# Kernel optimization log

Measured on AMD Instinct MI355X. Metric: run time of the kernel, lower is better.

## Reference

```python
import jax, jax.numpy as jnp
import numpy as np

B, NV, NRINGS, NDIRS, C, F = 2, 20000, 8, 8, 16, 16


def setup_inputs() -> dict:
    key = jax.random.key(0)
    ks = jax.random.split(key, 7)
    y = jax.random.normal(ks[0], (B, NV, NDIRS, C), jnp.float32)
    contributors = jax.random.randint(ks[1], (NV, NRINGS, NDIRS, 3), 0, NV, dtype=jnp.int32)
    weights_bary = jax.random.uniform(ks[2], (NV, NRINGS, NDIRS, 3), jnp.float32)
    angles = jax.random.randint(ks[3], (NV, NRINGS, NDIRS, 3), 0, NDIRS, dtype=jnp.int32)
    kernel = jax.random.normal(ks[4], (NRINGS, NDIRS, C, F), jnp.float32) * 0.05
    center_kernel = jax.random.normal(ks[5], (C, F), jnp.float32) * 0.05
    bias = jnp.zeros((F,), jnp.float32)
    return {"y": y, "contributors": contributors, "weights_bary": weights_bary,
            "angles": angles, "kernel": kernel, "center_kernel": center_kernel, "bias": bias}


def reference(y, contributors, weights_bary, angles, kernel, center_kernel, bias):
    # y: (B, nv, ndirs, C); tables: (nv, nrings, ndirs, 3)
    b, nv, ndirs, nch = y.shape
    nfilters = kernel.shape[-1]
    nrings = contributors.shape[1]

    # window_interpolation_sync: gather 3 contributor vertices per window bin,
    # with the direction axis re-indexed per-contributor (radial sync), then
    # barycentric-weighted sum.  Flatten (vertex, dir) into one gather index.
    idx = contributors * ndirs + angles                 # (nv, nrings, ndirs, 3)
    y_flat = y.reshape(b, nv * ndirs, nch)
    gathered = y_flat[:, idx, :]                        # (B, nv, nrings, ndirs, 3, C)
    z = jnp.einsum('bvrdjc,vrdj->bvrdc', gathered, weights_bary)  # (B, nv, nrings, ndirs, C)

    # gcnn_conv: circular pad over dirs then VALID conv with (nrings, ndirs) kernel
    zr = z.reshape(b * nv, nrings, ndirs, nch)
    zr = jnp.concatenate([zr, zr[:, :, :-1, :]], axis=2)  # width 2*ndirs-1
    conv = jax.lax.conv_general_dilated(
        zr, kernel, window_strides=(1, 1), padding='VALID',
        dimension_numbers=('NHWC', 'HWIO', 'NHWC'))       # (B*nv, 1, ndirs, F)
    conv = conv.reshape(b, nv, ndirs, nfilters)

    out = conv + jnp.einsum('bvdc,cf->bvdf', y, center_kernel) + bias
    out = jax.nn.relu(out)
    return jnp.max(out, axis=2)                          # take_max over directions -> (B, nv, F)
```

## Files before the change

### kernel.cpp

```cpp
#include <hip/hip_runtime.h>

typedef unsigned short u16;
typedef __attribute__((ext_vector_type(4))) unsigned int u32x4;
typedef __attribute__((ext_vector_type(4))) float f32x4;
typedef __attribute__((ext_vector_type(8))) __bf16 bf16x8;

constexpr int BATCH = 2;
constexpr int NV    = 20000;
constexpr int ND    = 8;
constexpr int CH    = 16;
constexpr int NF    = 16;
constexpr int NVD   = NV * ND;
constexpr int NCHUNK = 36;
constexpr int MTOT  = BATCH * NV;
constexpr int BSTR  = 40;
constexpr int KSPLIT_CH = 18;

constexpr size_t Y16_OFF_B = 0;
constexpr size_t K2C_OFF_B = 10240000;
constexpr size_t PB_OFF_B  = 10534912;

__device__ __forceinline__ u16 f2bf(float x) {
    unsigned int u = __float_as_uint(x);
    unsigned int r = (u + 0x7fffu + ((u >> 16) & 1u)) >> 16;
    return (u16)r;
}
__device__ __forceinline__ unsigned int pack2bf(float a, float b) {
    return (unsigned int)f2bf(a) | ((unsigned int)f2bf(b) << 16);
}

__global__ __launch_bounds__(256) void prep(const float* __restrict__ y,
                                            u16* __restrict__ y16) {
    int tid = blockIdx.x * 256 + threadIdx.x;
    const float4* src = (const float4*)(y + (size_t)tid * 16);
    float4 v0 = src[0], v1 = src[1], v2 = src[2], v3 = src[3];
    u32x4 lo = {pack2bf(v0.x, v0.y), pack2bf(v0.z, v0.w), pack2bf(v1.x, v1.y), pack2bf(v1.z, v1.w)};
    u32x4 hi = {pack2bf(v2.x, v2.y), pack2bf(v2.z, v2.w), pack2bf(v3.x, v3.y), pack2bf(v3.z, v3.w)};
    u16* yd = y16 + (size_t)tid * 16;
    *(u32x4*)(yd)     = lo;
    *(u32x4*)(yd + 8) = hi;
}

__global__ __launch_bounds__(256) void k2_build(const float* __restrict__ kern,
                                                const float* __restrict__ ck,
                                                u16* __restrict__ k2c) {
    int e = blockIdx.x * 256 + threadIdx.x;
    int i = e & 4095;
    int kc = e >> 12;
    int n = i >> 5, kk = i & 31;
    int k = kc * 32 + kk;
    int w = n >> 4, f = n & 15;
    float val;
    if (k < 1024) {
        int r = k >> 7, dd = (k >> 4) & 7, c = k & 15;
        int d = (dd - w) & 7;
        val = kern[((r * 8 + d) * 16 + c) * 16 + f];
    } else {
        int ke = k - 1024;
        int d = ke >> 4, c = ke & 15;
        val = (d == w) ? ck[c * 16 + f] : 0.f;
    }
    k2c[e] = f2bf(val);
}

__global__ __launch_bounds__(256) void fused_gather_gemm(const u16* __restrict__ y16,
                                                         const int* __restrict__ contrib,
                                                         const float* __restrict__ wbary,
                                                         const int* __restrict__ angles,
                                                         const u16* __restrict__ k2c,
                                                         float* __restrict__ pb) {
    __shared__ __align__(16) u16 Bb[2][128 * BSTR];
    const int t = threadIdx.x;
    const int s  = blockIdx.x & 1;
    const int kcBeg = s * KSPLIT_CH;
    const int kcEnd = kcBeg + KSPLIT_CH;
    const int w = t >> 6, lane = t & 63;
    const int lrow = lane & 15, lq = lane >> 4;
    const int s_p = lq >> 1;
    const int h8  = (lq & 1) * 8;
    const int m0 = (blockIdx.x >> 1) * 64;
    const int arow = m0 + w * 16 + lrow;
    const int b_p = (arow >= NV);
    const int v_p = arow - b_p * NV;
    const u16* __restrict__ yb = y16 + (size_t)b_p * NVD * CH + h8;
    const int mb0 = v_p * 192 + s_p * 3;
    const int sn = t >> 1, sh = (t & 1) * 16;

    int   ce0, ce1, ce2, ae0, ae1, ae2;  float we0, we1, we2;
    int   co0, co1, co2, ao0, ao1, ao2;  float wo0, wo1, wo2;
    u32x4 ge0, ge1, ge2;  float ve0, ve1, ve2;
    u32x4 go0, go1, go2;  float vo0, vo1, vo2;
    u32x4 bne0, bne1, bno0, bno1;

    f32x4 acc[8];
    #pragma unroll
    for (int nt = 0; nt < 8; ++nt) acc[nt] = (f32x4){0.f, 0.f, 0.f, 0.f};

#define META_ISSUE(S, KC_) { const int o_ = mb0 + (KC_) * 6;                       \
    c##S##0 = contrib[o_]; c##S##1 = contrib[o_ + 1]; c##S##2 = contrib[o_ + 2];   \
    a##S##0 = angles[o_];  a##S##1 = angles[o_ + 1];  a##S##2 = angles[o_ + 2];    \
    w##S##0 = wbary[o_];   w##S##1 = wbary[o_ + 1];   w##S##2 = wbary[o_ + 2]; }

#define G_ISSUE(S, KC_) {                                                          \
    if ((KC_) < 32) {                                                              \
        g##S##0 = *(const u32x4*)(yb + (size_t)((unsigned)c##S##0 * 128u +         \
                                                (unsigned)a##S##0 * 16u));         \
        g##S##1 = *(const u32x4*)(yb + (size_t)((unsigned)c##S##1 * 128u +         \
                                                (unsigned)a##S##1 * 16u));         \
        g##S##2 = *(const u32x4*)(yb + (size_t)((unsigned)c##S##2 * 128u +         \
                                                (unsigned)a##S##2 * 16u));         \
        v##S##0 = w##S##0; v##S##1 = w##S##1; v##S##2 = w##S##2;                   \
    } else {                                                                       \
        g##S##0 = *(const u32x4*)(yb + (size_t)((unsigned)v_p * 128u +             \
                                      (unsigned)(2 * ((KC_) - 32) + s_p) * 16u));  \
    } }

#define COMBINE(S, KC_, A_) {                                                      \
    if ((KC_) < 32) {                                                              \
        float ac_[8];                                                              \
        _Pragma("unroll") for (int x_ = 0; x_ < 8; ++x_) ac_[x_] = 0.f;            \
        _Pragma("unroll")                                                          \
        for (int q_ = 0; q_ < 4; ++q_) {                                           \
            unsigned u0_ = g##S##0[q_], u1_ = g##S##1[q_], u2_ = g##S##2[q_];      \
            ac_[2 * q_]     += v##S##0 * __uint_as_float(u0_ << 16);               \
            ac_[2 * q_ + 1] += v##S##0 * __uint_as_float(u0_ & 0xffff0000u);       \
            ac_[2 * q_]     += v##S##1 * __uint_as_float(u1_ << 16);               \
            ac_[2 * q_ + 1] += v##S##1 * __uint_as_float(u1_ & 0xffff0000u);       \
            ac_[2 * q_]     += v##S##2 * __uint_as_float(u2_ << 16);               \
            ac_[2 * q_ + 1] += v##S##2 * __uint_as_float(u2_ & 0xffff0000u);       \
        }                                                                          \
        u32x4 o_;                                                                  \
        _Pragma("unroll") for (int q_ = 0; q_ < 4; ++q_)                           \
            o_[q_] = pack2bf(ac_[2 * q_], ac_[2 * q_ + 1]);                        \
        A_ = *(bf16x8*)&o_;                                                        \
    } else { u32x4 o_ = g##S##0; A_ = *(bf16x8*)&o_; } }

    META_ISSUE(e, kcBeg); META_ISSUE(o, kcBeg + 1);
    {
        const u32x4* src = (const u32x4*)(k2c + (size_t)kcBeg * 4096 + sn * 32 + sh);
        u32x4 b0 = src[0], b1 = src[1];
        u16* dst = &Bb[0][sn * BSTR + sh];
        *(u32x4*)(dst)     = b0;
        *(u32x4*)(dst + 8) = b1;
    }
    G_ISSUE(e, kcBeg); META_ISSUE(e, kcBeg + 2);
    G_ISSUE(o, kcBeg + 1);
    {
        const u32x4* src = (const u32x4*)(k2c + (size_t)(kcBeg + 1) * 4096 + sn * 32 + sh);
        bno0 = src[0]; bno1 = src[1];
    }

    for (int p = 0; p < KSPLIT_CH / 2; ++p) {
        const int k0 = kcBeg + 2 * p, k1 = k0 + 1;

        __syncthreads();
        if (k0 + 2 < kcEnd) {
            const u32x4* src = (const u32x4*)(k2c + (size_t)(k0 + 2) * 4096 + sn * 32 + sh);
            bne0 = src[0]; bne1 = src[1];
        }
        bf16x8 aev;
        COMBINE(e, k0, aev);
        if (k0 + 2 < kcEnd) G_ISSUE(e, k0 + 2);
        if (k0 + 3 < kcEnd && k0 + 3 < 32) META_ISSUE(o, k0 + 3);
        {
            bf16x8 bf[8];
            #pragma unroll
            for (int nt = 0; nt < 8; ++nt)
                bf[nt] = *(const bf16x8*)(&Bb[0][(nt * 16 + lrow) * BSTR + lq * 8]);
            #pragma unroll
            for (int nt = 0; nt < 8; ++nt)
                acc[nt] = __builtin_amdgcn_mfma_f32_16x16x32_bf16(aev, bf[nt], acc[nt], 0, 0, 0);
        }
        {
            u16* dst = &Bb[1][sn * BSTR + sh];
            *(u32x4*)(dst)     = bno0;
            *(u32x4*)(dst + 8) = bno1;
        }

        __syncthreads();
        if (k1 + 2 < kcEnd) {
            const u32x4* src = (const u32x4*)(k2c + (size_t)(k1 + 2) * 4096 + sn * 32 + sh);
            bno0 = src[0]; bno1 = src[1];
        }
        bf16x8 aov;
        COMBINE(o, k1, aov);
        if (k1 + 2 < kcEnd) G_ISSUE(o, k1 + 2);
        if (k1 + 3 < kcEnd && k1 + 3 < 32) META_ISSUE(e, k1 + 3);
        {
            bf16x8 bf[8];
            #pragma unroll
            for (int nt = 0; nt < 8; ++nt)
                bf[nt] = *(const bf16x8*)(&Bb[1][(nt * 16 + lrow) * BSTR + lq * 8]);
            #pragma unroll
            for (int nt = 0; nt < 8; ++nt)
                acc[nt] = __builtin_amdgcn_mfma_f32_16x16x32_bf16(aov, bf[nt], acc[nt], 0, 0, 0);
        }
        if (k1 + 1 < kcEnd) {
            u16* dst = &Bb[0][sn * BSTR + sh];
            *(u32x4*)(dst)     = bne0;
            *(u32x4*)(dst + 8) = bne1;
        }
    }
#undef META_ISSUE
#undef G_ISSUE
#undef COMBINE

    float* pbs = pb + (size_t)(s * 128) * MTOT;
    #pragma unroll
    for (int nt = 0; nt < 8; ++nt) {
        *(f32x4*)(pbs + (size_t)(nt * 16 + lrow) * MTOT + m0 + w * 16 + lq * 4) = acc[nt];
    }
}

__global__ __launch_bounds__(256) void combine_max(const float* __restrict__ pb,
                                                   const float* __restrict__ bias,
                                                   float* __restrict__ out) {
    int tid = blockIdx.x * 256 + threadIdx.x;
    if (tid >= 2 * MTOT) return;
    int row = tid >> 1, half = tid & 1;
    const float* p0 = pb + row;
    const float* p1 = pb + (size_t)128 * MTOT + row;
    float bs[8], m[8];
    #pragma unroll
    for (int j = 0; j < 8; ++j) { bs[j] = bias[half * 8 + j]; m[j] = 0.f; }
    #pragma unroll
    for (int w = 0; w < 8; ++w) {
        #pragma unroll
        for (int j = 0; j < 8; ++j) {
            int n = w * 16 + half * 8 + j;
            float v = p0[(size_t)n * MTOT] + p1[(size_t)n * MTOT] + bs[j];
            m[j] = fmaxf(m[j], v);
        }
    }
    float4 o0 = {m[0], m[1], m[2], m[3]};
    float4 o1 = {m[4], m[5], m[6], m[7]};
    float* dst = out + (size_t)row * NF + half * 8;
    *(float4*)(dst)     = o0;
    *(float4*)(dst + 4) = o1;
}

extern "C" void kernel_launch(void* const* d_in, const int* in_sizes, int n_in,
                              void* d_out, int out_size, void* d_ws, size_t ws_size,
                              hipStream_t stream) {
    const float* y      = (const float*)d_in[0];
    const int*   contrib= (const int*)d_in[1];
    const float* wbary  = (const float*)d_in[2];
    const int*   angles = (const int*)d_in[3];
    const float* kern   = (const float*)d_in[4];
    const float* ck     = (const float*)d_in[5];
    const float* bias   = (const float*)d_in[6];
    float* out = (float*)d_out;

    u16*   y16 = (u16*)((char*)d_ws + Y16_OFF_B);
    u16*   k2c = (u16*)((char*)d_ws + K2C_OFF_B);
    float* pb  = (float*)((char*)d_ws + PB_OFF_B);

    prep<<<1250, 256, 0, stream>>>(y, y16);
    k2_build<<<(NCHUNK * 4096) / 256, 256, 0, stream>>>(kern, ck, k2c);
    fused_gather_gemm<<<2 * (MTOT / 64), 256, 0, stream>>>(y16, contrib, wbary, angles,
                                                           k2c, pb);
    combine_max<<<(2 * MTOT + 255) / 256, 256, 0, stream>>>(pb, bias, out);
}
```

Measured before the change: 249.8 us.

## Deepen gather prefetch to three stages and merge prep kernels into one launch

The gather pipeline in the fused gather-GEMM kernel moves from two to three rotating register sets. Gathers are issued three chunks ahead and metadata six chunks ahead, giving more time to hide the latency of the random y16 loads. The y bf16 conversion and weight-matrix build kernels are also merged into one launch that branches on block index, saving a kernel launch. The deeper pipeline costs more live registers, which could lower occupancy or cause spills.

```diff
diff --git a/kernel.cpp b/kernel.cpp
--- a/kernel.cpp
+++ b/kernel.cpp
@@ -15,6 +15,8 @@
 constexpr int MTOT  = BATCH * NV;
 constexpr int BSTR  = 40;
 constexpr int KSPLIT_CH = 18;
+constexpr int PREP_BLOCKS = 1250;
+constexpr int K2_BLOCKS   = (NCHUNK * 4096) / 256;
 
 constexpr size_t Y16_OFF_B = 0;
 constexpr size_t K2C_OFF_B = 10240000;
@@ -29,38 +31,40 @@
     return (unsigned int)f2bf(a) | ((unsigned int)f2bf(b) << 16);
 }
 
-__global__ __launch_bounds__(256) void prep(const float* __restrict__ y,
-                                            u16* __restrict__ y16) {
-    int tid = blockIdx.x * 256 + threadIdx.x;
-    const float4* src = (const float4*)(y + (size_t)tid * 16);
-    float4 v0 = src[0], v1 = src[1], v2 = src[2], v3 = src[3];
-    u32x4 lo = {pack2bf(v0.x, v0.y), pack2bf(v0.z, v0.w), pack2bf(v1.x, v1.y), pack2bf(v1.z, v1.w)};
-    u32x4 hi = {pack2bf(v2.x, v2.y), pack2bf(v2.z, v2.w), pack2bf(v3.x, v3.y), pack2bf(v3.z, v3.w)};
-    u16* yd = y16 + (size_t)tid * 16;
-    *(u32x4*)(yd)     = lo;
-    *(u32x4*)(yd + 8) = hi;
-}
-
-__global__ __launch_bounds__(256) void k2_build(const float* __restrict__ kern,
-                                                const float* __restrict__ ck,
-                                                u16* __restrict__ k2c) {
-    int e = blockIdx.x * 256 + threadIdx.x;
-    int i = e & 4095;
-    int kc = e >> 12;
-    int n = i >> 5, kk = i & 31;
-    int k = kc * 32 + kk;
-    int w = n >> 4, f = n & 15;
-    float val;
-    if (k < 1024) {
-        int r = k >> 7, dd = (k >> 4) & 7, c = k & 15;
-        int d = (dd - w) & 7;
-        val = kern[((r * 8 + d) * 16 + c) * 16 + f];
+__global__ __launch_bounds__(256) void prep_k2(const float* __restrict__ y,
+                                               u16* __restrict__ y16,
+                                               const float* __restrict__ kern,
+                                               const float* __restrict__ ck,
+                                               u16* __restrict__ k2c) {
+    int bid = blockIdx.x;
+    if (bid < PREP_BLOCKS) {
+        int tid = bid * 256 + threadIdx.x;
+        const float4* src = (const float4*)(y + (size_t)tid * 16);
+        float4 v0 = src[0], v1 = src[1], v2 = src[2], v3 = src[3];
+        u32x4 lo = {pack2bf(v0.x, v0.y), pack2bf(v0.z, v0.w), pack2bf(v1.x, v1.y), pack2bf(v1.z, v1.w)};
+        u32x4 hi = {pack2bf(v2.x, v2.y), pack2bf(v2.z, v2.w), pack2bf(v3.x, v3.y), pack2bf(v3.z, v3.w)};
+        u16* yd = y16 + (size_t)tid * 16;
+        *(u32x4*)(yd)     = lo;
+        *(u32x4*)(yd + 8) = hi;
     } else {
-        int ke = k - 1024;
-        int d = ke >> 4, c = ke & 15;
-        val = (d == w) ? ck[c * 16 + f] : 0.f;
-    }
-    k2c[e] = f2bf(val);
+        int e = (bid - PREP_BLOCKS) * 256 + threadIdx.x;
+        int i = e & 4095;
+        int kc = e >> 12;
+        int n = i >> 5, kk = i & 31;
+        int k = kc * 32 + kk;
+        int w = n >> 4, f = n & 15;
+        float val;
+        if (k < 1024) {
+            int r = k >> 7, dd = (k >> 4) & 7, c = k & 15;
+            int d = (dd - w) & 7;
+            val = kern[((r * 8 + d) * 16 + c) * 16 + f];
+        } else {
+            int ke = k - 1024;
+            int d = ke >> 4, c = ke & 15;
+            val = (d == w) ? ck[c * 16 + f] : 0.f;
+        }
+        k2c[e] = f2bf(val);
+    }
 }
 
 __global__ __launch_bounds__(256) void fused_gather_gemm(const u16* __restrict__ y16,
@@ -86,10 +90,9 @@
     const int mb0 = v_p * 192 + s_p * 3;
     const int sn = t >> 1, sh = (t & 1) * 16;
 
-    int   ce0, ce1, ce2, ae0, ae1, ae2;  float we0, we1, we2;
-    int   co0, co1, co2, ao0, ao1, ao2;  float wo0, wo1, wo2;
-    u32x4 ge0, ge1, ge2;  float ve0, ve1, ve2;
-    u32x4 go0, go1, go2;  float vo0, vo1, vo2;
+    int   cA0, cA1, cA2, aA0, aA1, aA2;  float wA0, wA1, wA2, vA0, vA1, vA2;  u32x4 gA0, gA1, gA2;
+    int   cB0, cB1, cB2, aB0, aB1, aB2;  float wB0, wB1, wB2, vB0, vB1, vB2;  u32x4 gB0, gB1, gB2;
+    int   cC0, cC1, cC2, aC0, aC1, aC2;  float wC0, wC1, wC2, vC0, vC1, vC2;  u32x4 gC0, gC1, gC2;
     u32x4 bne0, bne1, bno0, bno1;
 
     f32x4 acc[8];
@@ -135,7 +138,57 @@
         A_ = *(bf16x8*)&o_;                                                        \
     } else { u32x4 o_ = g##S##0; A_ = *(bf16x8*)&o_; } }
 
-    META_ISSUE(e, kcBeg); META_ISSUE(o, kcBeg + 1);
+#define CHUNK_EV(S, KC_) {                                                              \
+    __syncthreads();                                                                    \
+    if ((KC_) + 2 < kcEnd) {                                                            \
+        const u32x4* src_ = (const u32x4*)(k2c + (size_t)((KC_) + 2) * 4096 + sn * 32 + sh); \
+        bne0 = src_[0]; bne1 = src_[1];                                                 \
+    }                                                                                   \
+    bf16x8 av_;                                                                         \
+    COMBINE(S, KC_, av_);                                                               \
+    if ((KC_) + 3 < kcEnd) G_ISSUE(S, (KC_) + 3);                                       \
+    if ((KC_) + 6 < kcEnd && (KC_) + 6 < 32) META_ISSUE(S, (KC_) + 6);                  \
+    {   bf16x8 bf_[8];                                                                  \
+        _Pragma("unroll")                                                               \
+        for (int nt_ = 0; nt_ < 8; ++nt_)                                               \
+            bf_[nt_] = *(const bf16x8*)(&Bb[0][(nt_ * 16 + lrow) * BSTR + lq * 8]);     \
+        _Pragma("unroll")                                                               \
+        for (int nt_ = 0; nt_ < 8; ++nt_)                                               \
+            acc[nt_] = __builtin_amdgcn_mfma_f32_16x16x32_bf16(av_, bf_[nt_], acc[nt_], 0, 0, 0); \
+    }                                                                                   \
+    if ((KC_) + 1 < kcEnd) {                                                            \
+        u16* dst_ = &Bb[1][sn * BSTR + sh];                                             \
+        *(u32x4*)(dst_)     = bno0;                                                     \
+        *(u32x4*)(dst_ + 8) = bno1;                                                     \
+    } }
+
+#define CHUNK_OD(S, KC_) {                                                              \
+    __syncthreads();                                                                    \
+    if ((KC_) + 2 < kcEnd) {                                                            \
+        const u32x4* src_ = (const u32x4*)(k2c + (size_t)((KC_) + 2) * 4096 + sn * 32 + sh); \
+        bno0 = src_[0]; bno1 = src_[1];                                                 \
+    }                                                                                   \
+    bf16x8 av_;                                                                         \
+    COMBINE(S, KC_, av_);                                                               \
+    if ((KC_) + 3 < kcEnd) G_ISSUE(S, (KC_) + 3);                                       \
+    if ((KC_) + 6 < kcEnd && (KC_) + 6 < 32) META_ISSUE(S, (KC_) + 6);                  \
+    {   bf16x8 bf_[8];                                                                  \
+        _Pragma("unroll")                                                               \
+        for (int nt_ = 0; nt_ < 8; ++nt_)                                               \
+            bf_[nt_] = *(const bf16x8*)(&Bb[1][(nt_ * 16 + lrow) * BSTR + lq * 8]);     \
+        _Pragma("unroll")                                                               \
+        for (int nt_ = 0; nt_ < 8; ++nt_)                                               \
+            acc[nt_] = __builtin_amdgcn_mfma_f32_16x16x32_bf16(av_, bf_[nt_], acc[nt_], 0, 0, 0); \
+    }                                                                                   \
+    if ((KC_) + 1 < kcEnd) {                                                            \
+        u16* dst_ = &Bb[0][sn * BSTR + sh];                                             \
+        *(u32x4*)(dst_)     = bne0;                                                     \
+        *(u32x4*)(dst_ + 8) = bne1;                                                     \
+    } }
+
+    META_ISSUE(A, kcBeg + 0);
+    META_ISSUE(B, kcBeg + 1);
+    META_ISSUE(C, kcBeg + 2);
     {
         const u32x4* src = (const u32x4*)(k2c + (size_t)kcBeg * 4096 + sn * 32 + sh);
         u32x4 b0 = src[0], b1 = src[1];
@@ -143,67 +196,28 @@
         *(u32x4*)(dst)     = b0;
         *(u32x4*)(dst + 8) = b1;
     }
-    G_ISSUE(e, kcBeg); META_ISSUE(e, kcBeg + 2);
-    G_ISSUE(o, kcBeg + 1);
+    G_ISSUE(A, kcBeg + 0); META_ISSUE(A, kcBeg + 3);
+    G_ISSUE(B, kcBeg + 1); META_ISSUE(B, kcBeg + 4);
+    G_ISSUE(C, kcBeg + 2); META_ISSUE(C, kcBeg + 5);
     {
         const u32x4* src = (const u32x4*)(k2c + (size_t)(kcBeg + 1) * 4096 + sn * 32 + sh);
         bno0 = src[0]; bno1 = src[1];
     }
 
-    for (int p = 0; p < KSPLIT_CH / 2; ++p) {
-        const int k0 = kcBeg + 2 * p, k1 = k0 + 1;
-
-        __syncthreads();
-        if (k0 + 2 < kcEnd) {
-            const u32x4* src = (const u32x4*)(k2c + (size_t)(k0 + 2) * 4096 + sn * 32 + sh);
-            bne0 = src[0]; bne1 = src[1];
-        }
-        bf16x8 aev;
-        COMBINE(e, k0, aev);
-        if (k0 + 2 < kcEnd) G_ISSUE(e, k0 + 2);
-        if (k0 + 3 < kcEnd && k0 + 3 < 32) META_ISSUE(o, k0 + 3);
-        {
-            bf16x8 bf[8];
-            #pragma unroll
-            for (int nt = 0; nt < 8; ++nt)
-                bf[nt] = *(const bf16x8*)(&Bb[0][(nt * 16 + lrow) * BSTR + lq * 8]);
-            #pragma unroll
-            for (int nt = 0; nt < 8; ++nt)
-                acc[nt] = __builtin_amdgcn_mfma_f32_16x16x32_bf16(aev, bf[nt], acc[nt], 0, 0, 0);
-        }
-        {
-            u16* dst = &Bb[1][sn * BSTR + sh];
-            *(u32x4*)(dst)     = bno0;
-            *(u32x4*)(dst + 8) = bno1;
-        }
-
-        __syncthreads();
-        if (k1 + 2 < kcEnd) {
-            const u32x4* src = (const u32x4*)(k2c + (size_t)(k1 + 2) * 4096 + sn * 32 + sh);
-            bno0 = src[0]; bno1 = src[1];
-        }
-        bf16x8 aov;
-        COMBINE(o, k1, aov);
-        if (k1 + 2 < kcEnd) G_ISSUE(o, k1 + 2);
-        if (k1 + 3 < kcEnd && k1 + 3 < 32) META_ISSUE(e, k1 + 3);
-        {
-            bf16x8 bf[8];
-            #pragma unroll
-            for (int nt = 0; nt < 8; ++nt)
-                bf[nt] = *(const bf16x8*)(&Bb[1][(nt * 16 + lrow) * BSTR + lq * 8]);
-            #pragma unroll
-            for (int nt = 0; nt < 8; ++nt)
-                acc[nt] = __builtin_amdgcn_mfma_f32_16x16x32_bf16(aov, bf[nt], acc[nt], 0, 0, 0);
-        }
-        if (k1 + 1 < kcEnd) {
-            u16* dst = &Bb[0][sn * BSTR + sh];
-            *(u32x4*)(dst)     = bne0;
-            *(u32x4*)(dst + 8) = bne1;
-        }
+    for (int p = 0; p < 3; ++p) {
+        const int base = kcBeg + 6 * p;
+        CHUNK_EV(A, base + 0);
+        CHUNK_OD(B, base + 1);
+        CHUNK_EV(C, base + 2);
+        CHUNK_OD(A, base + 3);
+        CHUNK_EV(B, base + 4);
+        CHUNK_OD(C, base + 5);
     }
 #undef META_ISSUE
 #undef G_ISSUE
 #undef COMBINE
+#undef CHUNK_EV
+#undef CHUNK_OD
 
     float* pbs = pb + (size_t)(s * 128) * MTOT;
     #pragma unroll
@@ -255,8 +269,7 @@
     u16*   k2c = (u16*)((char*)d_ws + K2C_OFF_B);
     float* pb  = (float*)((char*)d_ws + PB_OFF_B);
 
-    prep<<<1250, 256, 0, stream>>>(y, y16);
-    k2_build<<<(NCHUNK * 4096) / 256, 256, 0, stream>>>(kern, ck, k2c);
+    prep_k2<<<PREP_BLOCKS + K2_BLOCKS, 256, 0, stream>>>(y, y16, kern, ck, k2c);
     fused_gather_gemm<<<2 * (MTOT / 64), 256, 0, stream>>>(y16, contrib, wbary, angles,
                                                            k2c, pb);
     combine_max<<<(2 * MTOT + 255) / 256, 256, 0, stream>>>(pb, bias, out);
```

New measurement: 239.8 us. -4.0%, faster.
